# Kernel optimization log

Hardware: AMD Instinct MI355X
Metric: run time of the kernel (lower is better)

## Reference

```python
import jax, jax.numpy as jnp
import numpy as np

DIM = 512
HEADS = 8
DIM_HEAD = 64
VID = (8, 32, 32)   # (frames, height, width)
KS = (3, 3, 3)      # odd kernel sizes
DIL = (1, 1, 1)


def _build_indices():
    F, H, W = VID
    kf, kh, kw = KS
    df, dh, dw = DIL
    pf, ph, pw = df * (kf - 1) // 2, dh * (kh - 1) // 2, dw * (kw - 1) // 2
    Fp, Hp, Wp = F + 2 * pf, H + 2 * ph, W + 2 * pw
    N = F * H * W
    ff, yy, xx = np.meshgrid(np.arange(F), np.arange(H), np.arange(W), indexing='ij')
    of, oy, ox = np.meshgrid(np.arange(kf) * df, np.arange(kh) * dh, np.arange(kw) * dw, indexing='ij')
    nf = ff[..., None, None, None] + of   # (F,H,W,kf,kh,kw) coords in padded volume
    ny = yy[..., None, None, None] + oy
    nx = xx[..., None, None, None] + ox
    nbr = ((nf * Hp + ny) * Wp + nx).reshape(N, -1)  # (N, K) flat indices into padded volume
    sf, sy, sx = nf - pf, ny - ph, nx - pw           # source coords in unpadded volume
    valid = (sf >= 0) & (sf < F) & (sy >= 0) & (sy < H) & (sx >= 0) & (sx < W)
    tok = np.where(valid, (sf * H + sy) * W + sx, N).reshape(N, -1)  # sentinel N = padding
    mask = np.arange(N)[:, None] < tok               # causal mask; sentinel N always masked
    mask = np.concatenate([np.zeros((N, 1), bool), mask], axis=1)    # bos column never masked
    return jnp.asarray(nbr), jnp.asarray(mask), ((pf, pf), (ph, ph), (pw, pw))

_NBR, _MASK, _PAD = _build_indices()


def setup_inputs() -> dict:
    key = jax.random.key(0)
    ks = jax.random.split(key, 6)
    F, H, W = VID
    n = F * H * W + 1
    inner = HEADS * DIM_HEAD
    s = DIM ** -0.5
    return {
        "x":     jax.random.normal(ks[0], (1, n, DIM), jnp.float32),
        "w_q":   jax.random.normal(ks[1], (DIM, inner), jnp.float32) * s,
        "w_kv":  jax.random.normal(ks[2], (DIM, 2 * inner), jnp.float32) * s,
        "w_th":  jax.random.normal(ks[3], (HEADS, HEADS), jnp.float32) * HEADS ** -0.5,
        "w_out": jax.random.normal(ks[4], (inner, DIM), jnp.float32) * inner ** -0.5,
        "b_out": jnp.zeros((DIM,), jnp.float32),
    }


def reference(x, w_q, w_kv, w_th, w_out, b_out):
    b, n, _ = x.shape
    F, H, W = VID
    N = F * H * W  # n == N + 1 (BOS token first)
    h, d = HEADS, DIM_HEAD
    q = x @ w_q
    k, v = jnp.split(x @ w_kv, 2, axis=-1)

    def heads(t):
        return t.reshape(b, n, h, d).transpose(0, 2, 1, 3).reshape(b * h, n, d)

    q = heads(q) * d ** -0.5
    k, v = heads(k), heads(v)
    q = q[:, 1:]
    k_bos, k = k[:, :1], k[:, 1:]
    v_bos, v = v[:, :1], v[:, 1:]

    def unfold(t):  # gather 3D local neighborhoods: (bh, N, d) -> (bh, N, K, d)
        vol = jnp.pad(t.reshape(b * h, F, H, W, d), ((0, 0),) + _PAD + ((0, 0),))
        return vol.reshape(b * h, -1, d)[:, _NBR]

    kj = jnp.concatenate([jnp.broadcast_to(k_bos[:, None], (b * h, N, 1, d)), unfold(k)], axis=2)
    vj = jnp.concatenate([jnp.broadcast_to(v_bos[:, None], (b * h, N, 1, d)), unfold(v)], axis=2)

    sim = jnp.einsum('bid,bijd->bij', q, kj)                  # (bh, N, K+1)
    sim = jnp.where(_MASK[None], jnp.finfo(sim.dtype).min, sim)
    attn = jax.nn.softmax(sim, axis=-1)                       # stable_softmax == shift-invariant softmax
    attn = jnp.einsum('gh,bhij->bgij', w_th, attn.reshape(b, h, N, -1)).reshape(b * h, N, -1)
    out = jnp.einsum('bij,bijd->bid', attn, vj)               # (bh, N, d)
    out = jnp.concatenate([v_bos, out], axis=1)               # prepend bos value passthrough
    out = out.reshape(b, h, n, d).transpose(0, 2, 1, 3).reshape(b, n, h * d)
    return out @ w_out + b_out
```

## Files before the change

### kernel.cpp

```cpp
#include <hip/hip_runtime.h>
#include <stdint.h>

#define DIMC 512
#define INNER 512
#define NHEADS 8
#define DHEAD 64
#define NTOK 8192
#define NSEQ 8193
#define MPAD 8320
#define QKV_COLS 1536

#define CONV_XT   (MPAD * DIMC / 4)
#define CONV_WQKV (QKV_COLS * DIMC)
#define CONV_WOUT (INNER * DIMC)
#define CONV_TOT  (CONV_XT + CONV_WQKV + CONV_WOUT)

typedef __attribute__((ext_vector_type(8))) short bf16x8;
typedef __attribute__((ext_vector_type(4))) float f32x4;
typedef __attribute__((ext_vector_type(8))) unsigned short u16x8;

__device__ __forceinline__ float bf2f(unsigned short u) {
  return __uint_as_float(((unsigned int)u) << 16);
}
__device__ __forceinline__ unsigned short f2bf(float f) {
  unsigned int x = __float_as_uint(f);
  unsigned int lsb = (x >> 16) & 1u;
  x += 0x7fffu + lsb;
  return (unsigned short)(x >> 16);
}

__device__ __forceinline__ void gload_lds16(const unsigned short* g, unsigned short* l) {
  __builtin_amdgcn_global_load_lds(
      (const __attribute__((address_space(1))) void*)g,
      (__attribute__((address_space(3))) void*)l, 16, 0, 0);
}

__global__ void k_conv(const float* __restrict__ x, const float* __restrict__ wq,
                       const float* __restrict__ wkv, const float* __restrict__ wout,
                       unsigned short* __restrict__ xb, unsigned short* __restrict__ wqkvT,
                       unsigned short* __restrict__ woutT) {
  const int gid = blockIdx.x * 256 + threadIdx.x;
  if (gid < CONV_XT) {
    const int idx = gid * 4;
    const int row = idx / DIMC;
    ushort4 o;
    if (row < NSEQ) {
      const float4 v = *(const float4*)(x + idx);
      o.x = f2bf(v.x); o.y = f2bf(v.y); o.z = f2bf(v.z); o.w = f2bf(v.w);
    } else {
      o.x = 0; o.y = 0; o.z = 0; o.w = 0;
    }
    *(ushort4*)(xb + idx) = o;
  } else if (gid < CONV_XT + CONV_WQKV) {
    const int idx = gid - CONV_XT;
    const int c = idx / DIMC, k = idx % DIMC;
    const float v = (c < INNER) ? wq[k * INNER + c] * 0.125f
                                : wkv[k * (2 * INNER) + (c - INNER)];
    wqkvT[idx] = f2bf(v);
  } else {
    const int idx = gid - CONV_XT - CONV_WQKV;
    const int c = idx / DIMC, k = idx % DIMC;
    woutT[idx] = f2bf(wout[k * DIMC + c]);
  }
}

template <int TN, int LDC, bool OUT_BF16>
__global__ __launch_bounds__(256)
void k_gemm(const unsigned short* __restrict__ A,
            const unsigned short* __restrict__ BT,
            void* __restrict__ C,
            const float* __restrict__ bias,
            int Mreal) {
  __shared__ unsigned short As[128 * 64];
  __shared__ unsigned short Bs[128 * 64];

  int flat;
  {
    const int nwg = (int)gridDim.x;
    const int q = nwg >> 3, r = nwg & 7;
    const int xcd = (int)blockIdx.x & 7, idx = (int)blockIdx.x >> 3;
    flat = (xcd < r ? xcd * (q + 1) : r * (q + 1) + (xcd - r) * q) + idx;
  }
  const int tm = flat / TN;
  const int tn = flat % TN;

  const int tid = (int)threadIdx.x;
  const int wave = tid >> 6;
  const int lane = tid & 63;
  const int wm = (wave >> 1) * 64;
  const int wn = (wave & 1) * 64;

  f32x4 acc[4][4];
#pragma unroll
  for (int m = 0; m < 4; ++m)
#pragma unroll
    for (int n = 0; n < 4; ++n) {
      acc[m][n][0] = 0.f; acc[m][n][1] = 0.f; acc[m][n][2] = 0.f; acc[m][n][3] = 0.f;
    }

  const size_t a_base = (size_t)tm * 128 * DIMC;
  const size_t b_base = (size_t)tn * 128 * DIMC;
  const int lrow = lane >> 3;
  const int lk = (lane & 7) * 8;

  for (int k0 = 0; k0 < DIMC; k0 += 64) {
    __syncthreads();
#pragma unroll
    for (int c = 0; c < 4; ++c) {
      const int rA = wave * 32 + c * 8;
      gload_lds16(A + a_base + (size_t)(rA + lrow) * DIMC + k0 + lk, &As[rA * 64]);
      gload_lds16(BT + b_base + (size_t)(rA + lrow) * DIMC + k0 + lk, &Bs[rA * 64]);
    }
    __syncthreads();

    const int fr = lane & 15;
    const int kg = (lane >> 4) * 8;
#pragma unroll
    for (int kk = 0; kk < 2; ++kk) {
      bf16x8 af[4], bfr[4];
#pragma unroll
      for (int m = 0; m < 4; ++m)
        af[m] = *(const bf16x8*)&As[(wm + m * 16 + fr) * 64 + kk * 32 + kg];
#pragma unroll
      for (int n = 0; n < 4; ++n)
        bfr[n] = *(const bf16x8*)&Bs[(wn + n * 16 + fr) * 64 + kk * 32 + kg];
#pragma unroll
      for (int m = 0; m < 4; ++m)
#pragma unroll
        for (int n = 0; n < 4; ++n)
          acc[m][n] = __builtin_amdgcn_mfma_f32_16x16x32_bf16(af[m], bfr[n], acc[m][n], 0, 0, 0);
    }
  }

  const int fr = lane & 15;
  const int rg = (lane >> 4) * 4;
#pragma unroll
  for (int m = 0; m < 4; ++m) {
#pragma unroll
    for (int r = 0; r < 4; ++r) {
      const int row = tm * 128 + wm + m * 16 + rg + r;
      if (row < Mreal) {
#pragma unroll
        for (int n = 0; n < 4; ++n) {
          const int col = tn * 128 + wn + n * 16 + fr;
          const float v = acc[m][n][r];
          if constexpr (OUT_BF16) {
            ((unsigned short*)C)[(size_t)row * LDC + col] = f2bf(v);
          } else {
            ((float*)C)[(size_t)row * LDC + col] = v + bias[col];
          }
        }
      }
    }
  }
}

__global__ __launch_bounds__(256)
void k_attn2(const unsigned short* __restrict__ qkv, const float* __restrict__ w_th,
             unsigned short* __restrict__ Ob) {
  const int bid = (int)blockIdx.x;
  const int blk = ((bid & 7) << 8) | (bid >> 3);
  const int t = (int)threadIdx.x;
  const int w = t >> 6;
  const int l = t & 63;
  const int i = blk * 4 + w;
  const int e = l & 7;
  const int gbase = l & 56;

  int my_pack = -1;
  {
    const int f = i >> 10, rr = i & 1023, y = rr >> 5, xx = rr & 31;
    const int a = l / 9, rem = l % 9, bb = rem / 3, cc = rem % 3;
    const int sf = f + a - 1, sy = y + bb - 1, sx = xx + cc - 1;
    if (l < 27 && (unsigned)sf < 8u && (unsigned)sy < 32u && (unsigned)sx < 32u) {
      const int tk = (sf << 10) | (sy << 5) | sx;
      if (tk <= i) my_pack = tk + 1;
    }
  }
  const unsigned long long mask0 = __ballot(my_pack >= 0);
  const int nval = __popcll(mask0);

  float qf[8];
  {
    const u16x8 q8 = *(const u16x8*)(qkv + (size_t)(i + 1) * QKV_COLS + l * 8);
#pragma unroll
    for (int u = 0; u < 8; ++u) qf[u] = bf2f(q8[u]);
  }

  float s[4] = {-1e30f, -1e30f, -1e30f, -1e30f};
  const unsigned short* kbase = qkv + INNER + l * 8;
  {
    const u16x8 k8 = *(const u16x8*)kbase;
    float p = 0.f;
#pragma unroll
    for (int u = 0; u < 8; ++u) p = fmaf(qf[u], bf2f(k8[u]), p);
    p += __shfl_xor(p, 1); p += __shfl_xor(p, 2); p += __shfl_xor(p, 4);
    if (e == 0) s[0] = p;
  }
  {
    unsigned long long mask = mask0;
    int lane_cur = (int)__builtin_ctzll(mask);
    mask &= mask - 1;
    const int src0 = __shfl(my_pack, lane_cur);
    u16x8 k_cur = *(const u16x8*)(kbase + (size_t)src0 * QKV_COLS);
    for (int it = 0; it < nval; ++it) {
      const int lane_nxt = mask ? (int)__builtin_ctzll(mask) : 0;
      mask &= mask - 1;
      const int src_nxt_raw = __shfl(my_pack, lane_nxt);
      const int src_nxt = src_nxt_raw < 0 ? 0 : src_nxt_raw;
      const u16x8 k_nxt = *(const u16x8*)(kbase + (size_t)src_nxt * QKV_COLS);
      float p = 0.f;
#pragma unroll
      for (int u = 0; u < 8; ++u) p = fmaf(qf[u], bf2f(k_cur[u]), p);
      p += __shfl_xor(p, 1); p += __shfl_xor(p, 2); p += __shfl_xor(p, 4);
      const int jslot = lane_cur + 1;
      const bool mine = (e == (jslot & 7));
      const int pp = jslot >> 3;
      s[0] = (mine && pp == 0) ? p : s[0];
      s[1] = (mine && pp == 1) ? p : s[1];
      s[2] = (mine && pp == 2) ? p : s[2];
      s[3] = (mine && pp == 3) ? p : s[3];
      k_cur = k_nxt; lane_cur = lane_nxt;
    }
  }

  float mx = fmaxf(fmaxf(s[0], s[1]), fmaxf(s[2], s[3]));
  mx = fmaxf(mx, __shfl_xor(mx, 1));
  mx = fmaxf(mx, __shfl_xor(mx, 2));
  mx = fmaxf(mx, __shfl_xor(mx, 4));
  float a4[4]; float sum = 0.f;
#pragma unroll
  for (int p = 0; p < 4; ++p) { a4[p] = __expf(s[p] - mx); sum += a4[p]; }
  sum += __shfl_xor(sum, 1); sum += __shfl_xor(sum, 2); sum += __shfl_xor(sum, 4);
  const float inv = 1.0f / sum;
#pragma unroll
  for (int p = 0; p < 4; ++p) a4[p] *= inv;

  float wth[8];
  {
    const float4 w0 = *(const float4*)(w_th + gbase);
    const float4 w1 = *(const float4*)(w_th + gbase + 4);
    wth[0] = w0.x; wth[1] = w0.y; wth[2] = w0.z; wth[3] = w0.w;
    wth[4] = w1.x; wth[5] = w1.y; wth[6] = w1.z; wth[7] = w1.w;
  }
  float m4[4];
#pragma unroll
  for (int p = 0; p < 4; ++p) {
    float acc = 0.f;
#pragma unroll
    for (int h2 = 0; h2 < 8; ++h2)
      acc = fmaf(wth[h2], __shfl(a4[p], (h2 << 3) | e), acc);
    m4[p] = acc;
  }

  float acc8[8] = {0.f, 0.f, 0.f, 0.f, 0.f, 0.f, 0.f, 0.f};
  const unsigned short* vbase = qkv + 2 * INNER + l * 8;
  {
    const float mv = __shfl(m4[0], gbase);
    const u16x8 v8 = *(const u16x8*)vbase;
#pragma unroll
    for (int u = 0; u < 8; ++u) acc8[u] = fmaf(mv, bf2f(v8[u]), acc8[u]);
  }
  {
    unsigned long long mask = mask0;
    int lane_cur = (int)__builtin_ctzll(mask);
    mask &= mask - 1;
    const int src0 = __shfl(my_pack, lane_cur);
    u16x8 v_cur = *(const u16x8*)(vbase + (size_t)src0 * QKV_COLS);
    for (int it = 0; it < nval; ++it) {
      const int lane_nxt = mask ? (int)__builtin_ctzll(mask) : 0;
      mask &= mask - 1;
      const int src_nxt_raw = __shfl(my_pack, lane_nxt);
      const int src_nxt = src_nxt_raw < 0 ? 0 : src_nxt_raw;
      const u16x8 v_nxt = *(const u16x8*)(vbase + (size_t)src_nxt * QKV_COLS);
      const int jslot = lane_cur + 1;
      const int pp = jslot >> 3;
      const float msel = pp == 0 ? m4[0] : pp == 1 ? m4[1] : pp == 2 ? m4[2] : m4[3];
      const float mv = __shfl(msel, gbase | (jslot & 7));
#pragma unroll
      for (int u = 0; u < 8; ++u) acc8[u] = fmaf(mv, bf2f(v_cur[u]), acc8[u]);
      v_cur = v_nxt; lane_cur = lane_nxt;
    }
  }

  u16x8 o;
#pragma unroll
  for (int u = 0; u < 8; ++u) o[u] = f2bf(acc8[u]);
  *(u16x8*)(Ob + (size_t)(i + 1) * INNER + l * 8) = o;
}

__global__ void k_bos(const unsigned short* __restrict__ qkv, unsigned short* __restrict__ Ob) {
  const int t = (int)(blockIdx.x * 256 + threadIdx.x);
  if (t < INNER) Ob[t] = qkv[2 * INNER + t];
}

extern "C" void kernel_launch(void* const* d_in, const int* in_sizes, int n_in,
                              void* d_out, int out_size, void* d_ws, size_t ws_size,
                              hipStream_t stream) {
  (void)in_sizes; (void)n_in; (void)out_size; (void)ws_size;
  const float* x     = (const float*)d_in[0];
  const float* w_q   = (const float*)d_in[1];
  const float* w_kv  = (const float*)d_in[2];
  const float* w_th  = (const float*)d_in[3];
  const float* w_out = (const float*)d_in[4];
  const float* b_out = (const float*)d_in[5];
  float* out = (float*)d_out;

  char* ws = (char*)d_ws;
  unsigned short* xb    = (unsigned short*)ws;
  unsigned short* wqkvT = (unsigned short*)(ws + 8519680);
  unsigned short* woutT = (unsigned short*)(ws + 8519680 + 1572864);
  unsigned short* qkvb  = (unsigned short*)(ws + 8519680 + 1572864 + 524288);

  k_conv<<<CONV_TOT / 256, 256, 0, stream>>>(x, w_q, w_kv, w_out, xb, wqkvT, woutT);
  k_gemm<QKV_COLS / 128, QKV_COLS, true><<<(MPAD / 128) * (QKV_COLS / 128), 256, 0, stream>>>(
      xb, wqkvT, qkvb, nullptr, NSEQ);
  k_attn2<<<NTOK / 4, 256, 0, stream>>>(qkvb, w_th, xb);
  k_bos<<<2, 256, 0, stream>>>(qkvb, xb);
  k_gemm<DIMC / 128, DIMC, false><<<(MPAD / 128) * (DIMC / 128), 256, 0, stream>>>(
      xb, woutT, out, b_out, NSEQ);
}
```

Measured before the change: 82.58 us.

## Unroll attention gather loops by two, fold BOS copy, narrow output GEMM tile

The attention kernel's K and V neighbor loops now handle two neighbors per iteration with independent loads and accumulators, replacing the single-step software prefetch. The goal is more memory-level parallelism and shorter dependency chains. The separate BOS-copy kernel is folded into an extra block of the attention kernel, saving one launch. The output projection GEMM uses a 128x64 tile, which doubles the workgroup count to improve occupancy of the small N=512 GEMM, at the cost of less B-tile reuse per block.

```diff
diff --git a/kernel.cpp b/kernel.cpp
--- a/kernel.cpp
+++ b/kernel.cpp
@@ -3,8 +3,6 @@
 
 #define DIMC 512
 #define INNER 512
-#define NHEADS 8
-#define DHEAD 64
 #define NTOK 8192
 #define NSEQ 8193
 #define MPAD 8320
@@ -64,7 +62,7 @@
   }
 }
 
-template <int TN, int LDC, bool OUT_BF16>
+template <int BN, int TN, int LDC, bool OUT_BF16>
 __global__ __launch_bounds__(256)
 void k_gemm(const unsigned short* __restrict__ A,
             const unsigned short* __restrict__ BT,
@@ -72,7 +70,9 @@
             const float* __restrict__ bias,
             int Mreal) {
   __shared__ unsigned short As[128 * 64];
-  __shared__ unsigned short Bs[128 * 64];
+  __shared__ unsigned short Bs[BN * 64];
+  constexpr int MF = (BN == 128) ? 4 : 2;
+  constexpr int ISS_B = BN / 32;
 
   int flat;
   {
@@ -87,19 +87,19 @@
   const int tid = (int)threadIdx.x;
   const int wave = tid >> 6;
   const int lane = tid & 63;
-  const int wm = (wave >> 1) * 64;
-  const int wn = (wave & 1) * 64;
-
-  f32x4 acc[4][4];
-#pragma unroll
-  for (int m = 0; m < 4; ++m)
+  const int wm = (BN == 128) ? ((wave >> 1) * 64) : (wave * 32);
+  const int wn = (BN == 128) ? ((wave & 1) * 64) : 0;
+
+  f32x4 acc[MF][4];
+#pragma unroll
+  for (int m = 0; m < MF; ++m)
 #pragma unroll
     for (int n = 0; n < 4; ++n) {
       acc[m][n][0] = 0.f; acc[m][n][1] = 0.f; acc[m][n][2] = 0.f; acc[m][n][3] = 0.f;
     }
 
   const size_t a_base = (size_t)tm * 128 * DIMC;
-  const size_t b_base = (size_t)tn * 128 * DIMC;
+  const size_t b_base = (size_t)tn * BN * DIMC;
   const int lrow = lane >> 3;
   const int lk = (lane & 7) * 8;
 
@@ -109,7 +109,11 @@
     for (int c = 0; c < 4; ++c) {
       const int rA = wave * 32 + c * 8;
       gload_lds16(A + a_base + (size_t)(rA + lrow) * DIMC + k0 + lk, &As[rA * 64]);
-      gload_lds16(BT + b_base + (size_t)(rA + lrow) * DIMC + k0 + lk, &Bs[rA * 64]);
+    }
+#pragma unroll
+    for (int c = 0; c < ISS_B; ++c) {
+      const int rB = wave * (BN / 4) + c * 8;
+      gload_lds16(BT + b_base + (size_t)(rB + lrow) * DIMC + k0 + lk, &Bs[rB * 64]);
     }
     __syncthreads();
 
@@ -117,15 +121,15 @@
     const int kg = (lane >> 4) * 8;
 #pragma unroll
     for (int kk = 0; kk < 2; ++kk) {
-      bf16x8 af[4], bfr[4];
-#pragma unroll
-      for (int m = 0; m < 4; ++m)
+      bf16x8 af[MF], bfr[4];
+#pragma unroll
+      for (int m = 0; m < MF; ++m)
         af[m] = *(const bf16x8*)&As[(wm + m * 16 + fr) * 64 + kk * 32 + kg];
 #pragma unroll
       for (int n = 0; n < 4; ++n)
         bfr[n] = *(const bf16x8*)&Bs[(wn + n * 16 + fr) * 64 + kk * 32 + kg];
 #pragma unroll
-      for (int m = 0; m < 4; ++m)
+      for (int m = 0; m < MF; ++m)
 #pragma unroll
         for (int n = 0; n < 4; ++n)
           acc[m][n] = __builtin_amdgcn_mfma_f32_16x16x32_bf16(af[m], bfr[n], acc[m][n], 0, 0, 0);
@@ -135,14 +139,14 @@
   const int fr = lane & 15;
   const int rg = (lane >> 4) * 4;
 #pragma unroll
-  for (int m = 0; m < 4; ++m) {
+  for (int m = 0; m < MF; ++m) {
 #pragma unroll
     for (int r = 0; r < 4; ++r) {
       const int row = tm * 128 + wm + m * 16 + rg + r;
       if (row < Mreal) {
 #pragma unroll
         for (int n = 0; n < 4; ++n) {
-          const int col = tn * 128 + wn + n * 16 + fr;
+          const int col = tn * BN + wn + n * 16 + fr;
           const float v = acc[m][n][r];
           if constexpr (OUT_BF16) {
             ((unsigned short*)C)[(size_t)row * LDC + col] = f2bf(v);
@@ -156,11 +160,15 @@
 }
 
 __global__ __launch_bounds__(256)
-void k_attn2(const unsigned short* __restrict__ qkv, const float* __restrict__ w_th,
+void k_attn3(const unsigned short* __restrict__ qkv, const float* __restrict__ w_th,
              unsigned short* __restrict__ Ob) {
   const int bid = (int)blockIdx.x;
+  const int t = (int)threadIdx.x;
+  if (bid == NTOK / 4) {
+    *(unsigned int*)(Ob + 2 * t) = *(const unsigned int*)(qkv + 2 * INNER + 2 * t);
+    return;
+  }
   const int blk = ((bid & 7) << 8) | (bid >> 3);
-  const int t = (int)threadIdx.x;
   const int w = t >> 6;
   const int l = t & 63;
   const int i = blk * 4 + w;
@@ -199,28 +207,44 @@
   }
   {
     unsigned long long mask = mask0;
-    int lane_cur = (int)__builtin_ctzll(mask);
-    mask &= mask - 1;
-    const int src0 = __shfl(my_pack, lane_cur);
-    u16x8 k_cur = *(const u16x8*)(kbase + (size_t)src0 * QKV_COLS);
-    for (int it = 0; it < nval; ++it) {
-      const int lane_nxt = mask ? (int)__builtin_ctzll(mask) : 0;
+    for (int it = 0; it < nval; it += 2) {
+      const int l0 = (int)__builtin_ctzll(mask);
       mask &= mask - 1;
-      const int src_nxt_raw = __shfl(my_pack, lane_nxt);
-      const int src_nxt = src_nxt_raw < 0 ? 0 : src_nxt_raw;
-      const u16x8 k_nxt = *(const u16x8*)(kbase + (size_t)src_nxt * QKV_COLS);
-      float p = 0.f;
-#pragma unroll
-      for (int u = 0; u < 8; ++u) p = fmaf(qf[u], bf2f(k_cur[u]), p);
-      p += __shfl_xor(p, 1); p += __shfl_xor(p, 2); p += __shfl_xor(p, 4);
-      const int jslot = lane_cur + 1;
-      const bool mine = (e == (jslot & 7));
-      const int pp = jslot >> 3;
-      s[0] = (mine && pp == 0) ? p : s[0];
-      s[1] = (mine && pp == 1) ? p : s[1];
-      s[2] = (mine && pp == 2) ? p : s[2];
-      s[3] = (mine && pp == 3) ? p : s[3];
-      k_cur = k_nxt; lane_cur = lane_nxt;
+      const bool has1 = (it + 1) < nval;
+      const int l1 = mask ? (int)__builtin_ctzll(mask) : 0;
+      mask &= mask - 1;
+      const int pk0 = __shfl(my_pack, l0);
+      const int pk1r = __shfl(my_pack, l1);
+      const int pk1 = has1 ? pk1r : 0;
+      const u16x8 ka = *(const u16x8*)(kbase + (size_t)pk0 * QKV_COLS);
+      const u16x8 kb = *(const u16x8*)(kbase + (size_t)pk1 * QKV_COLS);
+      float p0 = 0.f, p1 = 0.f;
+#pragma unroll
+      for (int u = 0; u < 8; ++u) {
+        p0 = fmaf(qf[u], bf2f(ka[u]), p0);
+        p1 = fmaf(qf[u], bf2f(kb[u]), p1);
+      }
+      p0 += __shfl_xor(p0, 1); p1 += __shfl_xor(p1, 1);
+      p0 += __shfl_xor(p0, 2); p1 += __shfl_xor(p1, 2);
+      p0 += __shfl_xor(p0, 4); p1 += __shfl_xor(p1, 4);
+      {
+        const int js = l0 + 1;
+        const bool mine = (e == (js & 7));
+        const int pp = js >> 3;
+        s[0] = (mine && pp == 0) ? p0 : s[0];
+        s[1] = (mine && pp == 1) ? p0 : s[1];
+        s[2] = (mine && pp == 2) ? p0 : s[2];
+        s[3] = (mine && pp == 3) ? p0 : s[3];
+      }
+      {
+        const int js = l1 + 1;
+        const bool mine = has1 && (e == (js & 7));
+        const int pp = js >> 3;
+        s[0] = (mine && pp == 0) ? p1 : s[0];
+        s[1] = (mine && pp == 1) ? p1 : s[1];
+        s[2] = (mine && pp == 2) ? p1 : s[2];
+        s[3] = (mine && pp == 3) ? p1 : s[3];
+      }
     }
   }
 
@@ -254,6 +278,7 @@
   }
 
   float acc8[8] = {0.f, 0.f, 0.f, 0.f, 0.f, 0.f, 0.f, 0.f};
+  float accb[8] = {0.f, 0.f, 0.f, 0.f, 0.f, 0.f, 0.f, 0.f};
   const unsigned short* vbase = qkv + 2 * INNER + l * 8;
   {
     const float mv = __shfl(m4[0], gbase);
@@ -263,35 +288,38 @@
   }
   {
     unsigned long long mask = mask0;
-    int lane_cur = (int)__builtin_ctzll(mask);
-    mask &= mask - 1;
-    const int src0 = __shfl(my_pack, lane_cur);
-    u16x8 v_cur = *(const u16x8*)(vbase + (size_t)src0 * QKV_COLS);
-    for (int it = 0; it < nval; ++it) {
-      const int lane_nxt = mask ? (int)__builtin_ctzll(mask) : 0;
+    for (int it = 0; it < nval; it += 2) {
+      const int l0 = (int)__builtin_ctzll(mask);
       mask &= mask - 1;
-      const int src_nxt_raw = __shfl(my_pack, lane_nxt);
-      const int src_nxt = src_nxt_raw < 0 ? 0 : src_nxt_raw;
-      const u16x8 v_nxt = *(const u16x8*)(vbase + (size_t)src_nxt * QKV_COLS);
-      const int jslot = lane_cur + 1;
-      const int pp = jslot >> 3;
-      const float msel = pp == 0 ? m4[0] : pp == 1 ? m4[1] : pp == 2 ? m4[2] : m4[3];
-      const float mv = __shfl(msel, gbase | (jslot & 7));
-#pragma unroll
-      for (int u = 0; u < 8; ++u) acc8[u] = fmaf(mv, bf2f(v_cur[u]), acc8[u]);
-      v_cur = v_nxt; lane_cur = lane_nxt;
+      const bool has1 = (it + 1) < nval;
+      const int l1 = mask ? (int)__builtin_ctzll(mask) : 0;
+      mask &= mask - 1;
+      const int pk0 = __shfl(my_pack, l0);
+      const int pk1r = __shfl(my_pack, l1);
+      const int pk1 = has1 ? pk1r : 0;
+      const u16x8 va = *(const u16x8*)(vbase + (size_t)pk0 * QKV_COLS);
+      const u16x8 vb = *(const u16x8*)(vbase + (size_t)pk1 * QKV_COLS);
+      const int js0 = l0 + 1;
+      const int pp0 = js0 >> 3;
+      const float ms0 = pp0 == 0 ? m4[0] : pp0 == 1 ? m4[1] : pp0 == 2 ? m4[2] : m4[3];
+      const float mv0 = __shfl(ms0, gbase | (js0 & 7));
+      const int js1 = l1 + 1;
+      const int pp1 = js1 >> 3;
+      const float ms1 = pp1 == 0 ? m4[0] : pp1 == 1 ? m4[1] : pp1 == 2 ? m4[2] : m4[3];
+      const float mv1r = __shfl(ms1, gbase | (js1 & 7));
+      const float mv1 = has1 ? mv1r : 0.f;
+#pragma unroll
+      for (int u = 0; u < 8; ++u) {
+        acc8[u] = fmaf(mv0, bf2f(va[u]), acc8[u]);
+        accb[u] = fmaf(mv1, bf2f(vb[u]), accb[u]);
+      }
     }
   }
 
   u16x8 o;
 #pragma unroll
-  for (int u = 0; u < 8; ++u) o[u] = f2bf(acc8[u]);
+  for (int u = 0; u < 8; ++u) o[u] = f2bf(acc8[u] + accb[u]);
   *(u16x8*)(Ob + (size_t)(i + 1) * INNER + l * 8) = o;
-}
-
-__global__ void k_bos(const unsigned short* __restrict__ qkv, unsigned short* __restrict__ Ob) {
-  const int t = (int)(blockIdx.x * 256 + threadIdx.x);
-  if (t < INNER) Ob[t] = qkv[2 * INNER + t];
 }
 
 extern "C" void kernel_launch(void* const* d_in, const int* in_sizes, int n_in,
@@ -313,10 +341,9 @@
   unsigned short* qkvb  = (unsigned short*)(ws + 8519680 + 1572864 + 524288);
 
   k_conv<<<CONV_TOT / 256, 256, 0, stream>>>(x, w_q, w_kv, w_out, xb, wqkvT, woutT);
-  k_gemm<QKV_COLS / 128, QKV_COLS, true><<<(MPAD / 128) * (QKV_COLS / 128), 256, 0, stream>>>(
-      xb, wqkvT, qkvb, nullptr, NSEQ);
-  k_attn2<<<NTOK / 4, 256, 0, stream>>>(qkvb, w_th, xb);
-  k_bos<<<2, 256, 0, stream>>>(qkvb, xb);
-  k_gemm<DIMC / 128, DIMC, false><<<(MPAD / 128) * (DIMC / 128), 256, 0, stream>>>(
-      xb, woutT, out, b_out, NSEQ);
-}
+  k_gemm<128, QKV_COLS / 128, QKV_COLS, true>
+      <<<(MPAD / 128) * (QKV_COLS / 128), 256, 0, stream>>>(xb, wqkvT, qkvb, nullptr, NSEQ);
+  k_attn3<<<NTOK / 4 + 1, 256, 0, stream>>>(qkvb, w_th, xb);
+  k_gemm<64, DIMC / 64, DIMC, false>
+      <<<(MPAD / 128) * (DIMC / 64), 256, 0, stream>>>(xb, woutT, out, b_out, NSEQ);
+}
```

Result: faster. 75.89 us (-8.1%).
